# Kernel optimization log

Measured on AMD Instinct MI355X. Metric: run time of the kernel, lower is better.

## Reference

```python
import jax, jax.numpy as jnp
import numpy as np

EMB = 1024
HEADS = 16
HEAD_DIM = EMB // HEADS
B, T = 2, 2048
EPS = 1e-5


def setup_inputs() -> dict:
    key = jax.random.key(0)
    ks = jax.random.split(key, 12)
    s_in = (1.0 / np.sqrt(EMB)).astype(np.float32)
    s_hid = (1.0 / np.sqrt(4 * EMB)).astype(np.float32)
    return {
        "x": jax.random.normal(ks[0], (B, T, EMB), jnp.float32),
        "Wq": jax.random.normal(ks[1], (HEADS, EMB, HEAD_DIM), jnp.float32) * s_in,
        "Wk": jax.random.normal(ks[2], (HEADS, EMB, HEAD_DIM), jnp.float32) * s_in,
        "Wv": jax.random.normal(ks[3], (HEADS, EMB, HEAD_DIM), jnp.float32) * s_in,
        "W1": jax.random.normal(ks[4], (EMB, 4 * EMB), jnp.float32) * s_in,
        "b1": jnp.zeros((4 * EMB,), jnp.float32),
        "W2": jax.random.normal(ks[5], (4 * EMB, EMB), jnp.float32) * s_hid,
        "b2": jnp.zeros((EMB,), jnp.float32),
        "g1": jnp.ones((EMB,), jnp.float32),
        "be1": jnp.zeros((EMB,), jnp.float32),
        "g2": jnp.ones((EMB,), jnp.float32),
        "be2": jnp.zeros((EMB,), jnp.float32),
    }


def _layernorm1d(x, gain, bias):
    # Faithful to source: normalize over dim 1 (sequence dim of [B,T,C]),
    # with UNBIASED variance (torch.var default).
    mean = jnp.mean(x, axis=1, keepdims=True)
    var = jnp.var(x, axis=1, keepdims=True, ddof=1)
    return gain * (x - mean) / jnp.sqrt(var + EPS) + bias


def _attention(x, Wq, Wk, Wv):
    Bq, Tq, C = x.shape
    q = jnp.einsum("btc,hcd->bhtd", x, Wq)
    k = jnp.einsum("btc,hcd->bhtd", x, Wk)
    v = jnp.einsum("btc,hcd->bhtd", x, Wv)
    # NOTE: scale uses input channel dim C (=emb_size), as in the source.
    wei = jnp.einsum("bhtd,bhsd->bhts", q, k) * (C ** -0.5)
    causal = jnp.tril(jnp.ones((Tq, Tq), bool))
    wei = jnp.where(causal, wei, -jnp.inf)
    wei = jax.nn.softmax(wei, axis=-1)
    out = jnp.einsum("bhts,bhsd->bhtd", wei, v)
    # concat over heads (dim=-1) == transpose + reshape
    return out.transpose(0, 2, 1, 3).reshape(Bq, Tq, -1)


def reference(x, Wq, Wk, Wv, W1, b1, W2, b2, g1, be1, g2, be2):
    x = x + _attention(_layernorm1d(x, g1, be1), Wq, Wk, Wv)
    h = _layernorm1d(x, g2, be2)
    h = jax.nn.relu(h @ W1 + b1) @ W2 + b2
    return x + h
```

## Files before the change

### kernel.cpp

```cpp
#include <hip/hip_runtime.h>


typedef __bf16 bf16x8 __attribute__((ext_vector_type(8)));
typedef float f32x4 __attribute__((ext_vector_type(4)));
typedef unsigned short u16;
typedef u16 u16x8 __attribute__((ext_vector_type(8)));
typedef u16 u16x4 __attribute__((ext_vector_type(4)));

#define MFMA16 __builtin_amdgcn_mfma_f32_16x16x32_bf16

__device__ __forceinline__ u16 f2bf(float f) {
  return __builtin_bit_cast(u16, (__bf16)f);
}
__device__ __forceinline__ float bf2f(u16 u) {
  return __builtin_bit_cast(float, (unsigned)u << 16);
}
__device__ __forceinline__ bf16x8 ldbf8(const u16* p) {
  return __builtin_bit_cast(bf16x8, *reinterpret_cast<const u16x8*>(p));
}
__device__ __forceinline__ void gll16(const void* g, void* l) {
  __builtin_amdgcn_global_load_lds((const __attribute__((address_space(1))) void*)g,
                                   (__attribute__((address_space(3))) void*)l, 16, 0, 0);
}
template <int N>
__device__ __forceinline__ void wait_vm() {
  if constexpr (N == 0)      asm volatile("s_waitcnt vmcnt(0)" ::: "memory");
  else if constexpr (N == 6) asm volatile("s_waitcnt vmcnt(6)" ::: "memory");
  else if constexpr (N == 8) asm volatile("s_waitcnt vmcnt(8)" ::: "memory");
  else                       asm volatile("s_waitcnt vmcnt(16)" ::: "memory");
}
__device__ __forceinline__ void barrier_raw() {
  asm volatile("" ::: "memory");
  __builtin_amdgcn_s_barrier();
  asm volatile("" ::: "memory");
}
__device__ __forceinline__ int qb_off(int qb) {
  if (qb < 8)  return qb;
  if (qb < 16) return 8 + (qb - 8) * 2;
  if (qb < 24) return 24 + (qb - 16) * 3;
  return 48 + (qb - 24) * 4;
}

__global__ __launch_bounds__(256) void prep_fused(const float* __restrict__ Wq,
                                                  const float* __restrict__ Wk,
                                                  const float* __restrict__ Wv,
                                                  const float* __restrict__ W1,
                                                  const float* __restrict__ W2,
                                                  const float* __restrict__ x,
                                                  u16* __restrict__ wqkvt,
                                                  u16* __restrict__ w1t,
                                                  u16* __restrict__ w2t,
                                                  float2* __restrict__ part,
                                                  float scale) {
  __shared__ alignas(16) char smem[64 * 65 * 4];
  const int id = blockIdx.x;
  if (id < 2816) {
    const float* in;
    u16* out;
    int K, N, kb, nb, roff = 0;
    float sc = 1.0f;
    if (id < 768) {
      const int z = id >> 8, rem = id & 255;
      in = z == 0 ? Wq : (z == 1 ? Wk : Wv);
      if (z == 0) sc = scale;
      out = wqkvt;
      K = 1024; N = 64;
      kb = rem & 15; nb = 0;
      roff = z * 1024 + (rem >> 4) * 64;
      in += (size_t)(rem >> 4) * 1024 * 64;
    } else if (id < 1792) {
      const int i2 = id - 768;
      in = W1; out = w1t; K = 1024; N = 4096; kb = i2 & 15; nb = i2 >> 4;
    } else {
      const int i2 = id - 1792;
      in = W2; out = w2t; K = 4096; N = 1024; kb = i2 >> 4; nb = i2 & 15;
    }
    float (*tile)[65] = (float(*)[65])smem;
    const int k0 = kb * 64, n0 = nb * 64;
    const int c = threadIdx.x & 63, rg = threadIdx.x >> 6;
#pragma unroll
    for (int i = 0; i < 16; ++i) {
      int r = rg * 16 + i;
      tile[r][c] = in[(size_t)(k0 + r) * N + n0 + c];
    }
    __syncthreads();
#pragma unroll
    for (int i = 0; i < 16; ++i) {
      int nl = rg * 16 + i;
      out[(size_t)(roff + n0 + nl) * K + k0 + c] = f2bf(tile[c][nl] * sc);
    }
  } else {
    const int idm = id - 2816;
    const int bx = idm & 31, by = idm >> 5;
    const int b = bx >> 4, c0 = (bx & 15) * 64;
    const int c = c0 + (threadIdx.x & 63), tg = threadIdx.x >> 6;
    const int t0 = by * 256 + tg * 64;
    float s = 0.f, sq = 0.f;
    const float* p = x + (size_t)(b * 2048 + t0) * 1024 + c;
#pragma unroll 8
    for (int i = 0; i < 64; ++i) {
      float v = p[(size_t)i * 1024];
      s += v; sq += v * v;
    }
    float* ss = (float*)smem;
    float* sb = ss + 256;
    ss[threadIdx.x] = s; sb[threadIdx.x] = sq;
    __syncthreads();
    if (threadIdx.x < 64) {
      s  = ss[threadIdx.x] + ss[threadIdx.x + 64] + ss[threadIdx.x + 128] + ss[threadIdx.x + 192];
      sq = sb[threadIdx.x] + sb[threadIdx.x + 64] + sb[threadIdx.x + 128] + sb[threadIdx.x + 192];
      part[(size_t)(b * 1024 + c) * 8 + by] = make_float2(s, sq);
    }
  }
}

template <int NC>
__global__ __launch_bounds__(256) void ln_stats_apply(const float* __restrict__ x,
                                                      const float2* __restrict__ part,
                                                      const float* __restrict__ g,
                                                      const float* __restrict__ be,
                                                      u16* __restrict__ out) {
  const int slab = blockIdx.x * 64;
  const int y0 = blockIdx.y * 256;
  const int b = blockIdx.z;
  const int tid = threadIdx.x;
  __shared__ float2 sst[64];
  __shared__ float sg[64], sbe[64];
  if (tid < 64) {
    const int c = slab + tid;
    float s = 0.f, sq = 0.f;
#pragma unroll
    for (int i = 0; i < NC; ++i) {
      float2 v = part[(size_t)(b * 1024 + c) * NC + i];
      s += v.x; sq += v.y;
    }
    const float mean = s * (1.0f / 2048.0f);
    const float var = (sq - 2048.0f * mean * mean) * (1.0f / 2047.0f);
    sst[tid] = make_float2(mean, rsqrtf(var + 1e-5f));
    sg[tid] = g[c];
    sbe[tid] = be[c];
  }
  __syncthreads();
  const int c4 = (tid & 15) * 4;
  const int r0 = tid >> 4;
  const size_t base = ((size_t)(b * 2048 + y0)) * 1024 + slab + c4;
#pragma unroll
  for (int it = 0; it < 16; ++it) {
    const int row = r0 * 16 + it;
    float4 xv = *reinterpret_cast<const float4*>(x + base + (size_t)row * 1024);
    float vs[4] = {xv.x, xv.y, xv.z, xv.w};
    u16x4 o;
#pragma unroll
    for (int j = 0; j < 4; ++j) {
      float2 st = sst[c4 + j];
      o[j] = f2bf(sg[c4 + j] * (vs[j] - st.x) * st.y + sbe[c4 + j]);
    }
    *reinterpret_cast<u16x4*>(out + base + (size_t)row * 1024) = o;
  }
}

template <int WTN, int EPI>
__device__ __forceinline__ void gemm_core(const u16* __restrict__ A,
                                          const u16* __restrict__ Bt,
                                          u16* __restrict__ outb,
                                          float* __restrict__ outf,
                                          const float* __restrict__ bias,
                                          const float* __restrict__ resid,
                                          int N, int K, int m0, int n0) {
  constexpr int BM = 128, BN = 2 * WTN;
  constexpr int NI = WTN / 16;
  constexpr int BCH = BN / 8;
  constexpr int LPW = (16 + BCH) / 4;
  __shared__ alignas(16) u16 sA[2][BM * 64];
  __shared__ alignas(16) u16 sB[2][BN * 64];
  const int tid = threadIdx.x, lane = tid & 63, wid = tid >> 6;
  const int wm = (wid >> 1) * 64, wn = (wid & 1) * WTN;
  const int lr = lane & 15, lg = lane >> 4;
  const int srow = lane >> 3;
  const int sgr = (lane & 7) ^ srow;
  const int x7 = lr & 7;
  f32x4 acc[4][NI] = {};

  auto stage = [&](int buf, int k0) {
#pragma unroll
    for (int i = 0; i < LPW; ++i) {
      const int c = wid * LPW + i;
      if (c < 16) {
        const int r = c * 8 + srow;
        gll16(A + (size_t)(m0 + r) * K + k0 + sgr * 8, &sA[buf][c * 512]);
      } else {
        const int r = (c - 16) * 8 + srow;
        gll16(Bt + (size_t)(n0 + r) * K + k0 + sgr * 8, &sB[buf][(c - 16) * 512]);
      }
    }
  };

  const int nsteps = K >> 6;
  stage(0, 0);
  int cur = 0;
  for (int t = 0; t < nsteps; ++t) {
    if (t + 1 < nsteps) {
      stage(cur ^ 1, (t + 1) * 64);
      wait_vm<LPW>();
    } else {
      wait_vm<0>();
    }
    barrier_raw();
    bf16x8 af[4][2], bfr[NI][2];
#pragma unroll
    for (int mi = 0; mi < 4; ++mi)
#pragma unroll
      for (int kk = 0; kk < 2; ++kk)
        af[mi][kk] = ldbf8(&sA[cur][(wm + mi * 16 + lr) * 64 + (((kk * 4 + lg) ^ x7) * 8)]);
#pragma unroll
    for (int ni = 0; ni < NI; ++ni)
#pragma unroll
      for (int kk = 0; kk < 2; ++kk)
        bfr[ni][kk] = ldbf8(&sB[cur][(wn + ni * 16 + lr) * 64 + (((kk * 4 + lg) ^ x7) * 8)]);
#pragma unroll
    for (int kk = 0; kk < 2; ++kk)
#pragma unroll
      for (int mi = 0; mi < 4; ++mi)
#pragma unroll
        for (int ni = 0; ni < NI; ++ni)
          acc[mi][ni] = MFMA16(af[mi][kk], bfr[ni][kk], acc[mi][ni], 0, 0, 0);
    barrier_raw();
    cur ^= 1;
  }

#pragma unroll
  for (int mi = 0; mi < 4; ++mi)
#pragma unroll
    for (int ni = 0; ni < NI; ++ni)
#pragma unroll
      for (int r = 0; r < 4; ++r) {
        const int row = m0 + wm + mi * 16 + lg * 4 + r;
        const int col = n0 + wn + ni * 16 + lr;
        float v = acc[mi][ni][r];
        if (EPI == 0) {
          outb[(size_t)row * N + col] = f2bf(v);
        } else if (EPI == 1) {
          v += bias[col];
          v = fmaxf(v, 0.f);
          outb[(size_t)row * N + col] = f2bf(v);
        } else {
          v += bias[col] + resid[(size_t)row * N + col];
          outf[(size_t)row * N + col] = v;
        }
      }
}

template <int WTN, int EPI, int MINW>
__global__ __launch_bounds__(256, MINW) void gemm_kernel(const u16* __restrict__ A,
                                                         const u16* __restrict__ Bt,
                                                         u16* __restrict__ outb,
                                                         float* __restrict__ outf,
                                                         const float* __restrict__ bias,
                                                         const float* __restrict__ resid,
                                                         int N, int K) {
  constexpr int BN = 2 * WTN;
  const int gx = gridDim.x;
  const int nwg = gx * gridDim.y;
  int bid = blockIdx.y * gx + blockIdx.x;
  bid = (bid & 7) * (nwg >> 3) + (bid >> 3);
  const int n0 = (bid % gx) * BN, m0 = (bid / gx) * 128;
  gemm_core<WTN, EPI>(A, Bt, outb, outf, bias, resid, N, K, m0, n0);
}

__global__ __launch_bounds__(256, 2) void gemm_qkvt(const u16* __restrict__ hbuf,
                                                    const u16* __restrict__ wqkvt,
                                                    u16* __restrict__ qkb,
                                                    u16* __restrict__ vtb) {
  int bid = blockIdx.x;
  const u16 *A, *Bt;
  u16* outb;
  int N, m0, n0;
  if (bid < 512) {
    bid = (bid & 7) * 64 + (bid >> 3);
    A = hbuf; Bt = wqkvt; outb = qkb; N = 2048;
    n0 = (bid % 16) * 128; m0 = (bid / 16) * 128;
  } else {
    int b2 = bid - 512;
    b2 = (b2 & 7) * 32 + (b2 >> 3);
    A = wqkvt + 2048 * 1024; Bt = hbuf; outb = vtb; N = 4096;
    n0 = (b2 % 32) * 128; m0 = (b2 / 32) * 128;
  }
  gemm_core<64, 0>(A, Bt, outb, nullptr, nullptr, nullptr, N, 1024, m0, n0);
}

__global__ __launch_bounds__(256) void attn_partial(const u16* __restrict__ qk,
                                                    const u16* __restrict__ vt,
                                                    u16* __restrict__ Opart,
                                                    float2* __restrict__ ml) {
  const int xr = 79 - (int)blockIdx.x;
  int qb, ch, nc;
  if (xr < 8)       { qb = xr;                ch = 0;            nc = 1; }
  else if (xr < 24) { qb = 8 + ((xr - 8) >> 1);  ch = (xr - 8) & 1;  nc = 2; }
  else if (xr < 48) { qb = 16 + (xr - 24) / 3;   ch = (xr - 24) % 3; nc = 3; }
  else              { qb = 24 + ((xr - 48) >> 2); ch = (xr - 48) & 3; nc = 4; }
  const int nt_tot = qb + 1;
  const int t0 = (ch * nt_tot) / nc;
  const int t1 = ((ch + 1) * nt_tot) / nc;
  const int bh = blockIdx.y, b = bh >> 4, h = bh & 15;
  const int slot = bh * 80 + xr;
  const int q0 = qb * 64;
  const int tid = threadIdx.x, lane = tid & 63, w = tid >> 6;
  const int lr = lane & 15, lg = lane >> 4;
  __shared__ alignas(16) u16 sK[64 * 64];
  __shared__ alignas(16) u16 sV[64 * 64];
  __shared__ alignas(16) u16 sP[4][16 * 64];

  const size_t qrow = (size_t)(b * 2048 + q0 + w * 16 + lr) * 2048 + h * 64;
  const bf16x8 aq0 = ldbf8(qk + qrow + lg * 8);
  const bf16x8 aq1 = ldbf8(qk + qrow + 32 + lg * 8);

  float m_i[4], l_i[4];
  f32x4 acc[4];
#pragma unroll
  for (int r = 0; r < 4; ++r) { m_i[r] = -1e30f; l_i[r] = 0.f; }
#pragma unroll
  for (int dn = 0; dn < 4; ++dn) acc[dn] = f32x4{0.f, 0.f, 0.f, 0.f};

  auto stage = [&](int s0) {
#pragma unroll
    for (int i = 0; i < 2; ++i) {
      const int c = w * 2 + i;
      const int g = c * 64 + lane;
      const int row = g >> 3;
      const int cs = (g & 7) ^ (row & 7);
      gll16(qk + (size_t)(b * 2048 + s0 + row) * 2048 + 1024 + h * 64 + cs * 8,
            &sK[c * 512]);
      gll16(vt + (size_t)(h * 64 + row) * 4096 + b * 2048 + s0 + cs * 8,
            &sV[c * 512]);
    }
  };

  for (int t = t0; t < t1; ++t) {
    stage(t * 64);
    wait_vm<0>();
    barrier_raw();

    f32x4 sf[4];
    __builtin_amdgcn_s_setprio(1);
#pragma unroll
    for (int sn = 0; sn < 4; ++sn) {
      const int row = sn * 16 + lr;
      const int x7 = lr & 7;
      bf16x8 k0f = ldbf8(&sK[row * 64 + ((lg ^ x7) * 8)]);
      bf16x8 k1f = ldbf8(&sK[row * 64 + (((4 + lg) ^ x7) * 8)]);
      f32x4 z = {0.f, 0.f, 0.f, 0.f};
      z = MFMA16(aq0, k0f, z, 0, 0, 0);
      z = MFMA16(aq1, k1f, z, 0, 0, 0);
      sf[sn] = z;
    }
    __builtin_amdgcn_s_setprio(0);

    if (t == nt_tot - 1) {
      const int qlb = w * 16 + lg * 4;
#pragma unroll
      for (int sn = 0; sn < 4; ++sn)
#pragma unroll
        for (int r = 0; r < 4; ++r)
          if (sn * 16 + lr > qlb + r) sf[sn][r] = -1e30f;
    }

    float pm[4];
    bool need = false;
#pragma unroll
    for (int r = 0; r < 4; ++r) {
      pm[r] = fmaxf(fmaxf(sf[0][r], sf[1][r]), fmaxf(sf[2][r], sf[3][r]));
      need = need || (pm[r] > m_i[r] + 8.f);
    }
    if (__any(need)) {
#pragma unroll
      for (int r = 0; r < 4; ++r) {
        float mx = pm[r];
        mx = fmaxf(mx, __shfl_xor(mx, 1, 16));
        mx = fmaxf(mx, __shfl_xor(mx, 2, 16));
        mx = fmaxf(mx, __shfl_xor(mx, 4, 16));
        mx = fmaxf(mx, __shfl_xor(mx, 8, 16));
        const float mnew = fmaxf(m_i[r], mx);
        const float al = exp2f(m_i[r] - mnew);
        l_i[r] *= al;
        acc[0][r] *= al; acc[1][r] *= al; acc[2][r] *= al; acc[3][r] *= al;
        m_i[r] = mnew;
      }
    }

    const int x7p = lr & 7;
#pragma unroll
    for (int r = 0; r < 4; ++r) {
      const float p0 = exp2f(sf[0][r] - m_i[r]), p1 = exp2f(sf[1][r] - m_i[r]);
      const float p2 = exp2f(sf[2][r] - m_i[r]), p3 = exp2f(sf[3][r] - m_i[r]);
      l_i[r] += (p0 + p1) + (p2 + p3);
      const int prow = lg * 4 + r;
      const int pb = prow * 64, px = prow & 7;
      sP[w][pb + (((lr >> 3) ^ px) * 8) + (lr & 7)]       = f2bf(p0);
      sP[w][pb + (((2 + (lr >> 3)) ^ px) * 8) + (lr & 7)] = f2bf(p1);
      sP[w][pb + (((4 + (lr >> 3)) ^ px) * 8) + (lr & 7)] = f2bf(p2);
      sP[w][pb + (((6 + (lr >> 3)) ^ px) * 8) + (lr & 7)] = f2bf(p3);
    }

    const bf16x8 pa0 = ldbf8(&sP[w][lr * 64 + ((lg ^ x7p) * 8)]);
    const bf16x8 pa1 = ldbf8(&sP[w][lr * 64 + (((4 + lg) ^ x7p) * 8)]);
    __builtin_amdgcn_s_setprio(1);
#pragma unroll
    for (int dn = 0; dn < 4; ++dn) {
      const int row = dn * 16 + lr;
      bf16x8 v0f = ldbf8(&sV[row * 64 + ((lg ^ x7p) * 8)]);
      bf16x8 v1f = ldbf8(&sV[row * 64 + (((4 + lg) ^ x7p) * 8)]);
      acc[dn] = MFMA16(pa0, v0f, acc[dn], 0, 0, 0);
      acc[dn] = MFMA16(pa1, v1f, acc[dn], 0, 0, 0);
    }
    __builtin_amdgcn_s_setprio(0);
    barrier_raw();
  }

  const int rbase = w * 16 + lg * 4;
#pragma unroll
  for (int r = 0; r < 4; ++r) {
    float ls = l_i[r];
    ls += __shfl_xor(ls, 1, 16);
    ls += __shfl_xor(ls, 2, 16);
    ls += __shfl_xor(ls, 4, 16);
    ls += __shfl_xor(ls, 8, 16);
    const int row = rbase + r;
    if (lr == 0) ml[(size_t)slot * 64 + row] = make_float2(m_i[r], ls);
#pragma unroll
    for (int dn = 0; dn < 4; ++dn)
      Opart[((size_t)slot * 64 + row) * 64 + dn * 16 + lr] = f2bf(acc[dn][r]);
  }
}

__global__ __launch_bounds__(256) void attn_merge_ln(const u16* __restrict__ Opart,
                                                     const float2* __restrict__ ml,
                                                     const float* __restrict__ x,
                                                     float* __restrict__ x2,
                                                     float2* __restrict__ part) {
  const int qb = blockIdx.x, bh = blockIdx.y, b = bh >> 4, h = bh & 15;
  const int nc = (qb >> 3) + 1;
  const size_t slot0 = (size_t)bh * 80 + qb_off(qb);
  const int tid = threadIdx.x;
  const int row = tid >> 2, d0 = (tid & 3) * 16;
  __shared__ float red[64][65];

  float wgt[4];
  float mmax = -1e30f, lsum = 0.f;
  for (int i = 0; i < nc; ++i) {
    float2 v = ml[(slot0 + i) * 64 + row];
    wgt[i] = v.x;
    mmax = fmaxf(mmax, v.x);
  }
  for (int i = 0; i < nc; ++i) {
    float2 v = ml[(slot0 + i) * 64 + row];
    wgt[i] = exp2f(wgt[i] - mmax);
    lsum += wgt[i] * v.y;
  }
  const float inv = 1.0f / lsum;

#pragma unroll
  for (int half = 0; half < 2; ++half) {
    const int d = d0 + half * 8;
    float o[8] = {0.f, 0.f, 0.f, 0.f, 0.f, 0.f, 0.f, 0.f};
    for (int i = 0; i < nc; ++i) {
      u16x8 v = *reinterpret_cast<const u16x8*>(&Opart[((slot0 + i) * 64 + row) * 64 + d]);
#pragma unroll
      for (int jj = 0; jj < 8; ++jj) o[jj] += wgt[i] * bf2f(v[jj]);
    }
    const size_t idx = ((size_t)(b * 2048 + qb * 64 + row)) * 1024 + h * 64 + d;
    float4 x0 = *reinterpret_cast<const float4*>(x + idx);
    float4 x1 = *reinterpret_cast<const float4*>(x + idx + 4);
    float4 o0 = make_float4(x0.x + o[0] * inv, x0.y + o[1] * inv, x0.z + o[2] * inv, x0.w + o[3] * inv);
    float4 o1 = make_float4(x1.x + o[4] * inv, x1.y + o[5] * inv, x1.z + o[6] * inv, x1.w + o[7] * inv);
    *reinterpret_cast<float4*>(x2 + idx) = o0;
    *reinterpret_cast<float4*>(x2 + idx + 4) = o1;
    red[row][d + 0] = o0.x; red[row][d + 1] = o0.y; red[row][d + 2] = o0.z; red[row][d + 3] = o0.w;
    red[row][d + 4] = o1.x; red[row][d + 5] = o1.y; red[row][d + 6] = o1.z; red[row][d + 7] = o1.w;
  }
  __syncthreads();
  if (tid < 64) {
    float s = 0.f, sq = 0.f;
#pragma unroll 8
    for (int t = 0; t < 64; ++t) {
      float v = red[t][tid];
      s += v; sq += v * v;
    }
    part[(size_t)(b * 1024 + h * 64 + tid) * 32 + qb] = make_float2(s, sq);
  }
}

extern "C" void kernel_launch(void* const* d_in, const int* in_sizes, int n_in,
                              void* d_out, int out_size, void* d_ws, size_t ws_size,
                              hipStream_t stream) {
  const float* x   = (const float*)d_in[0];
  const float* Wq  = (const float*)d_in[1];
  const float* Wk  = (const float*)d_in[2];
  const float* Wv  = (const float*)d_in[3];
  const float* W1  = (const float*)d_in[4];
  const float* b1  = (const float*)d_in[5];
  const float* W2  = (const float*)d_in[6];
  const float* b2  = (const float*)d_in[7];
  const float* g1  = (const float*)d_in[8];
  const float* be1 = (const float*)d_in[9];
  const float* g2  = (const float*)d_in[10];
  const float* be2 = (const float*)d_in[11];
  float* out = (float*)d_out;

  char* ws = (char*)d_ws;
  size_t off = 0;
  auto alloc = [&](size_t bytes) { char* p = ws + off; off += (bytes + 255) & ~(size_t)255; return p; };
  u16*    qkb   = (u16*)alloc(4096ull * 2048 * 2);
  u16*    vtb   = (u16*)alloc(1024ull * 4096 * 2);
  (void)alloc(4096ull * 1024 * 2);
  u16*    h1    = qkb;
  float*  x2    = (float*)alloc(4096ull * 1024 * 4);
  u16*    hbuf  = (u16*)alloc(4096ull * 1024 * 2);
  u16*    wqkvt = (u16*)alloc(3072ull * 1024 * 2);
  u16*    w1t   = (u16*)alloc(4096ull * 1024 * 2);
  u16*    w2t   = (u16*)alloc(1024ull * 4096 * 2);
  float2* part  = (float2*)alloc(2048ull * 32 * 8);
  float2* stats = (float2*)alloc(2048ull * 8);
  u16*    Opart = (u16*)alloc(32ull * 80 * 64 * 64 * 2);
  float2* ml    = (float2*)alloc(32ull * 80 * 64 * 8);
  (void)ws_size; (void)in_sizes; (void)n_in; (void)out_size; (void)stats;

  const float SC = 0.03125f * 1.44269504088896341f;
  prep_fused<<<3072, 256, 0, stream>>>(Wq, Wk, Wv, W1, W2, x, wqkvt, w1t, w2t, part, SC);

  ln_stats_apply<8><<<dim3(16, 8, 2), 256, 0, stream>>>(x, part, g1, be1, hbuf);

  gemm_qkvt<<<768, 256, 0, stream>>>(hbuf, wqkvt, qkb, vtb);

  attn_partial<<<dim3(80, 32), 256, 0, stream>>>(qkb, vtb, Opart, ml);
  attn_merge_ln<<<dim3(32, 32), 256, 0, stream>>>(Opart, ml, x, x2, part);

  ln_stats_apply<32><<<dim3(16, 8, 2), 256, 0, stream>>>(x2, part, g2, be2, hbuf);

  gemm_kernel<64, 1, 2><<<dim3(32, 32), 256, 0, stream>>>(hbuf, w1t, h1, nullptr, b1, nullptr, 4096, 1024);

  gemm_kernel<32, 2, 3><<<dim3(16, 32), 256, 0, stream>>>(h1, w2t, nullptr, out, b2, x2, 1024, 4096);
}
```

Before: 223.4 us.

## Fuse single-chunk attention blocks directly into residual and LN stats

Query blocks whose attention is handled by one chunk (first 8 qb) now normalize their output in the partial kernel, add the residual, write x2, and compute column sum/sumsq partials for the second layernorm. This skips writing and re-reading their Opart/ml partials, so the merge kernel launches only 24 query-block columns instead of 32. Shared memory is merged into one buffer so it can be reused for the stats reduction. A launch bound of 6 blocks per SM is also added, which may restrict registers.

```diff
diff --git a/kernel.cpp b/kernel.cpp
--- a/kernel.cpp
+++ b/kernel.cpp
@@ -288,10 +288,13 @@
   gemm_core<64, 0>(A, Bt, outb, nullptr, nullptr, nullptr, N, 1024, m0, n0);
 }
 
-__global__ __launch_bounds__(256) void attn_partial(const u16* __restrict__ qk,
-                                                    const u16* __restrict__ vt,
-                                                    u16* __restrict__ Opart,
-                                                    float2* __restrict__ ml) {
+__global__ __launch_bounds__(256, 6) void attn_partial(const u16* __restrict__ qk,
+                                                       const u16* __restrict__ vt,
+                                                       const float* __restrict__ x,
+                                                       float* __restrict__ x2,
+                                                       u16* __restrict__ Opart,
+                                                       float2* __restrict__ ml,
+                                                       float2* __restrict__ part) {
   const int xr = 79 - (int)blockIdx.x;
   int qb, ch, nc;
   if (xr < 8)       { qb = xr;                ch = 0;            nc = 1; }
@@ -306,9 +309,10 @@
   const int q0 = qb * 64;
   const int tid = threadIdx.x, lane = tid & 63, w = tid >> 6;
   const int lr = lane & 15, lg = lane >> 4;
-  __shared__ alignas(16) u16 sK[64 * 64];
-  __shared__ alignas(16) u16 sV[64 * 64];
-  __shared__ alignas(16) u16 sP[4][16 * 64];
+  __shared__ alignas(16) char smem[24576];
+  u16* const sK = (u16*)smem;
+  u16* const sV = (u16*)(smem + 8192);
+  u16* const sPw = (u16*)(smem + 16384) + w * (16 * 64);
 
   const size_t qrow = (size_t)(b * 2048 + q0 + w * 16 + lr) * 2048 + h * 64;
   const bf16x8 aq0 = ldbf8(qk + qrow + lg * 8);
@@ -395,14 +399,14 @@
       l_i[r] += (p0 + p1) + (p2 + p3);
       const int prow = lg * 4 + r;
       const int pb = prow * 64, px = prow & 7;
-      sP[w][pb + (((lr >> 3) ^ px) * 8) + (lr & 7)]       = f2bf(p0);
-      sP[w][pb + (((2 + (lr >> 3)) ^ px) * 8) + (lr & 7)] = f2bf(p1);
-      sP[w][pb + (((4 + (lr >> 3)) ^ px) * 8) + (lr & 7)] = f2bf(p2);
-      sP[w][pb + (((6 + (lr >> 3)) ^ px) * 8) + (lr & 7)] = f2bf(p3);
-    }
-
-    const bf16x8 pa0 = ldbf8(&sP[w][lr * 64 + ((lg ^ x7p) * 8)]);
-    const bf16x8 pa1 = ldbf8(&sP[w][lr * 64 + (((4 + lg) ^ x7p) * 8)]);
+      sPw[pb + (((lr >> 3) ^ px) * 8) + (lr & 7)]       = f2bf(p0);
+      sPw[pb + (((2 + (lr >> 3)) ^ px) * 8) + (lr & 7)] = f2bf(p1);
+      sPw[pb + (((4 + (lr >> 3)) ^ px) * 8) + (lr & 7)] = f2bf(p2);
+      sPw[pb + (((6 + (lr >> 3)) ^ px) * 8) + (lr & 7)] = f2bf(p3);
+    }
+
+    const bf16x8 pa0 = ldbf8(&sPw[lr * 64 + ((lg ^ x7p) * 8)]);
+    const bf16x8 pa1 = ldbf8(&sPw[lr * 64 + (((4 + lg) ^ x7p) * 8)]);
     __builtin_amdgcn_s_setprio(1);
 #pragma unroll
     for (int dn = 0; dn < 4; ++dn) {
@@ -417,18 +421,49 @@
   }
 
   const int rbase = w * 16 + lg * 4;
-#pragma unroll
-  for (int r = 0; r < 4; ++r) {
-    float ls = l_i[r];
-    ls += __shfl_xor(ls, 1, 16);
-    ls += __shfl_xor(ls, 2, 16);
-    ls += __shfl_xor(ls, 4, 16);
-    ls += __shfl_xor(ls, 8, 16);
-    const int row = rbase + r;
-    if (lr == 0) ml[(size_t)slot * 64 + row] = make_float2(m_i[r], ls);
-#pragma unroll
-    for (int dn = 0; dn < 4; ++dn)
-      Opart[((size_t)slot * 64 + row) * 64 + dn * 16 + lr] = f2bf(acc[dn][r]);
+  if (nc == 1) {
+    float* fbuf = (float*)smem;
+#pragma unroll
+    for (int r = 0; r < 4; ++r) {
+      float ls = l_i[r];
+      ls += __shfl_xor(ls, 1, 16);
+      ls += __shfl_xor(ls, 2, 16);
+      ls += __shfl_xor(ls, 4, 16);
+      ls += __shfl_xor(ls, 8, 16);
+      const float inv = 1.0f / ls;
+      const int row = rbase + r;
+#pragma unroll
+      for (int dn = 0; dn < 4; ++dn) {
+        const size_t idx = ((size_t)(b * 2048 + q0 + row)) * 1024 + h * 64 + dn * 16 + lr;
+        const float val = x[idx] + acc[dn][r] * inv;
+        x2[idx] = val;
+        fbuf[row * 65 + dn * 16 + lr] = val;
+      }
+    }
+    __syncthreads();
+    if (tid < 64) {
+      float s = 0.f, sq = 0.f;
+#pragma unroll 8
+      for (int t2 = 0; t2 < 64; ++t2) {
+        float v = fbuf[t2 * 65 + tid];
+        s += v; sq += v * v;
+      }
+      part[(size_t)(b * 1024 + h * 64 + tid) * 32 + qb] = make_float2(s, sq);
+    }
+  } else {
+#pragma unroll
+    for (int r = 0; r < 4; ++r) {
+      float ls = l_i[r];
+      ls += __shfl_xor(ls, 1, 16);
+      ls += __shfl_xor(ls, 2, 16);
+      ls += __shfl_xor(ls, 4, 16);
+      ls += __shfl_xor(ls, 8, 16);
+      const int row = rbase + r;
+      if (lr == 0) ml[(size_t)slot * 64 + row] = make_float2(m_i[r], ls);
+#pragma unroll
+      for (int dn = 0; dn < 4; ++dn)
+        Opart[((size_t)slot * 64 + row) * 64 + dn * 16 + lr] = f2bf(acc[dn][r]);
+    }
   }
 }
 
@@ -437,7 +472,8 @@
                                                      const float* __restrict__ x,
                                                      float* __restrict__ x2,
                                                      float2* __restrict__ part) {
-  const int qb = blockIdx.x, bh = blockIdx.y, b = bh >> 4, h = bh & 15;
+  const int qb = 8 + (int)blockIdx.x;
+  const int bh = blockIdx.y, b = bh >> 4, h = bh & 15;
   const int nc = (qb >> 3) + 1;
   const size_t slot0 = (size_t)bh * 80 + qb_off(qb);
   const int tid = threadIdx.x;
@@ -531,8 +567,8 @@
 
   gemm_qkvt<<<768, 256, 0, stream>>>(hbuf, wqkvt, qkb, vtb);
 
-  attn_partial<<<dim3(80, 32), 256, 0, stream>>>(qkb, vtb, Opart, ml);
-  attn_merge_ln<<<dim3(32, 32), 256, 0, stream>>>(Opart, ml, x, x2, part);
+  attn_partial<<<dim3(80, 32), 256, 0, stream>>>(qkb, vtb, x, x2, Opart, ml, part);
+  attn_merge_ln<<<dim3(24, 32), 256, 0, stream>>>(Opart, ml, x, x2, part);
 
   ln_stats_apply<32><<<dim3(16, 8, 2), 256, 0, stream>>>(x2, part, g2, be2, hbuf);
 
```

Measured after the change: 251.4 us. +12.6%, slower.
